# Kernel tuning notes

Measured on AMD Instinct MI355X. Metric: run time of the kernel, lower is better.

## Reference

```python
import jax, jax.numpy as jnp
import numpy as np

E = 400000
N = 100000
B = 64
D = 128          # token_dim
H = 128          # hidden_dim
A = 2 * H        # action_dim


def setup_inputs() -> dict:
    key = jax.random.key(0)
    ks = jax.random.split(key, 12)
    inp = {
        "relation_tokens": jax.random.normal(ks[0], (E, D), jnp.float32),
        "node_tokens": jax.random.normal(ks[1], (N, D), jnp.float32),
        "edge_index": jax.random.randint(ks[2], (2, E), 0, N, jnp.int64 if jax.config.jax_enable_x64 else jnp.int32),
        "question_tokens": jax.random.normal(ks[3], (B, D), jnp.float32),
        "edge_batch": jax.random.randint(ks[4], (E,), 0, B, jnp.int64 if jax.config.jax_enable_x64 else jnp.int32),
        # learned params (xavier-like small init); stored as [in, out] for x @ W
        "W_rel": jax.random.normal(ks[5], (D, H), jnp.float32) * 0.05,
        "W_node": jax.random.normal(ks[6], (D, H), jnp.float32) * 0.05,
        "W_qgate": jax.random.normal(ks[7], (D, A), jnp.float32) * 0.05,
        "W_mlp1": jax.random.normal(ks[8], (A, A), jnp.float32) * 0.05,
        "b_mlp1": jnp.zeros((A,), jnp.float32),
        "W_mlp2": jax.random.normal(ks[9], (A, A), jnp.float32) * 0.05,
        "b_mlp2": jnp.zeros((A,), jnp.float32),
    }
    return inp


def reference(relation_tokens, node_tokens, edge_index, question_tokens, edge_batch,
              W_rel, W_node, W_qgate, W_mlp1, b_mlp1, W_mlp2, b_mlp2):
    # TrajectoryAgent.precompute_action_keys (dropout=0 -> identity)
    tail_nodes = edge_index[1]                       # [E]
    tail_tokens = node_tokens[tail_nodes]            # gather -> [E, D]
    q_tokens = question_tokens[edge_batch]           # gather -> [E, D]

    rel_key = relation_tokens @ W_rel                # [E, H]
    node_key = tail_tokens @ W_node                  # [E, H]
    q_gate = jax.nn.sigmoid(q_tokens @ W_qgate)      # [E, 2H]

    action_key = jnp.concatenate((rel_key, node_key), axis=-1) * q_gate  # [E, 2H]

    # action_mlp: Linear -> exact GELU -> Linear (torch nn.GELU default = erf)
    h = jax.nn.gelu(action_key @ W_mlp1 + b_mlp1, approximate=False)
    return h @ W_mlp2 + b_mlp2                       # [E, 2H]
```

## Files before the change

kernel.cpp:

```cpp
#include <hip/hip_runtime.h>

typedef __bf16 bf16;
typedef bf16 bf16x4 __attribute__((ext_vector_type(4)));
typedef bf16 bf16x8 __attribute__((ext_vector_type(8)));
typedef float f32x4 __attribute__((ext_vector_type(4)));

#define WS_PK1   0
#define WS_PK2   32768
#define WS_PK3   98304
#define WS_QG    163840

__global__ void prep_weights(const float* __restrict__ Wrel,
                             const float* __restrict__ Wnode,
                             const float* __restrict__ W1,
                             const float* __restrict__ W2,
                             bf16* __restrict__ ws) {
  int id = blockIdx.x * 256 + threadIdx.x;
  if (id < 32768) {
    int cg = id >> 13, rem = id & 8191;
    int kk = rem >> 11;
    int ai = (rem >> 9) & 3;
    int l  = (rem >> 3) & 63;
    int j  = rem & 7;
    int n  = (cg & 1) * 64 + ai * 16 + (l & 15);
    int k  = kk * 32 + (l >> 4) * 8 + j;
    const float* src = (cg >> 1) ? Wnode : Wrel;
    ws[WS_PK1 + id] = (bf16)src[k * 128 + n];
  } else if (id < 98304) {
    int t = id - 32768;
    int cg = t >> 14, rem = t & 16383;
    int kk = rem >> 11;
    int ai = (rem >> 9) & 3;
    int l  = (rem >> 3) & 63;
    int j  = rem & 7;
    int n  = cg * 64 + ai * 16 + (l & 15);
    int k  = kk * 32 + (l >> 4) * 8 + j;
    ws[WS_PK2 + t] = (bf16)W1[k * 256 + n];
  } else if (id < 163840) {
    int t = id - 98304;
    int cg = t >> 14, rem = t & 16383;
    int kk = rem >> 11;
    int ai = (rem >> 9) & 3;
    int l  = (rem >> 3) & 63;
    int j  = rem & 7;
    int n  = cg * 64 + ai * 16 + (l & 15);
    int k  = kk * 32 + (l >> 4) * 8 + j;
    ws[WS_PK3 + t] = (bf16)W2[k * 256 + n];
  }
}

__global__ void prep_qg(const float* __restrict__ question,
                        const float* __restrict__ Wq,
                        bf16* __restrict__ qg) {
  int b = blockIdx.x, c = threadIdx.x;
  float s = 0.f;
#pragma unroll 8
  for (int k = 0; k < 128; ++k) s += question[b * 128 + k] * Wq[k * 256 + c];
  qg[b * 256 + c] = (bf16)(1.f / (1.f + expf(-s)));
}

__device__ __forceinline__ float gelu_fast(float x) {
  float x2 = x * x;
  float p = fmaf(0.0356774081f, x2, 0.7978845608f);
  float y = p * x;
  float e = __expf(2.f * y);
  float r = __builtin_amdgcn_rcpf(e + 1.f);
  float th = 1.f - 2.f * r;
  return 0.5f * x * (1.f + th);
}

typedef __attribute__((address_space(1))) const void gq_t;
typedef __attribute__((address_space(3))) void lq_t;
#define GLD16(g, s) __builtin_amdgcn_global_load_lds((gq_t*)(g), (lq_t*)(s), 16, 0, 0)
#define SBF() __builtin_amdgcn_sched_barrier(0xF)
#define SB7() __builtin_amdgcn_sched_barrier(0x7)
#define WAIT_VM0()   { asm volatile("s_waitcnt vmcnt(0)" ::: "memory"); SBF(); }
#define WAIT_LGKM0() { asm volatile("s_waitcnt lgkmcnt(0)" ::: "memory"); SBF(); }
#define VMWAIT(u)    { if ((u) <= 77)      { asm volatile("s_waitcnt vmcnt(2)" ::: "memory"); } \
                       else if ((u) == 78) { asm volatile("s_waitcnt vmcnt(1)" ::: "memory"); } \
                       else                { asm volatile("s_waitcnt vmcnt(0)" ::: "memory"); } \
                       SBF(); }
#define BAR() __builtin_amdgcn_s_barrier()

__global__ __launch_bounds__(256, 3) void fused_main(
    const float* __restrict__ rel_tok,
    const float* __restrict__ node_tok,
    const int*   __restrict__ tail_idx,
    const int*   __restrict__ ebatch,
    const bf16*  __restrict__ pk1,
    const bf16*  __restrict__ pk2,
    const bf16*  __restrict__ pk3,
    const bf16*  __restrict__ qg,
    const float* __restrict__ b1,
    const float* __restrict__ b2,
    float* __restrict__ out)
{
  __shared__ char  s_buf[32768];
  __shared__ char  s_w[16384];
  __shared__ float s_bias[512];

  const int tid = threadIdx.x;
  const int cg  = tid >> 6;
  const int l   = tid & 63;
  const int lo  = l & 15;
  const int hi  = l >> 4;
  const int base = blockIdx.x * 64;
  const int h1  = cg >> 1;

  auto issue_sub = [&](int u) {
    const bf16* g;
    if (u < 16)      g = pk1 + cg * 8192  + u * 512;
    else if (u < 48) g = pk2 + cg * 16384 + (u - 16) * 512;
    else             g = pk3 + cg * 16384 + (u - 48) * 512;
    GLD16(g + l * 8, s_w + (u & 3) * 4096 + cg * 1024 + l * 16);
  };

  int ebv[4];
#pragma unroll
  for (int bj = 0; bj < 4; ++bj) ebv[bj] = ebatch[base + bj * 16 + lo];
  bf16x4 gv[4][4];
#pragma unroll
  for (int bj = 0; bj < 4; ++bj)
#pragma unroll
    for (int ai = 0; ai < 4; ++ai)
      gv[bj][ai] = *(const bf16x4*)(qg + ebv[bj] * 256 + cg * 64 + ai * 16 + hi * 4);
  s_bias[tid]       = b1[tid];
  s_bias[256 + tid] = b2[tid];

  {
    const float4* g = (const float4*)rel_tok + (size_t)base * 32;
#pragma unroll
    for (int i = 0; i < 8; ++i) {
      int idx = tid + i * 256;
      int row = idx >> 5, c4 = idx & 31;
      float4 v = g[idx];
      bf16x4 b; b[0] = (bf16)v.x; b[1] = (bf16)v.y; b[2] = (bf16)v.z; b[3] = (bf16)v.w;
      int off = row * 256 + ((c4 * 8) ^ ((row & 15) << 4));
      *(bf16x4*)(s_buf + off) = b;
    }
#pragma unroll
    for (int i = 0; i < 8; ++i) {
      int idx = tid + i * 256;
      int row = idx >> 5, c4 = idx & 31;
      int tail = tail_idx[base + row];
      float4 v = ((const float4*)node_tok)[(size_t)tail * 32 + c4];
      bf16x4 b; b[0] = (bf16)v.x; b[1] = (bf16)v.y; b[2] = (bf16)v.z; b[3] = (bf16)v.w;
      int off = 16384 + row * 256 + ((c4 * 8) ^ ((row & 15) << 4));
      *(bf16x4*)(s_buf + off) = b;
    }
  }

  WAIT_VM0();
  issue_sub(0);
  issue_sub(1);
  issue_sub(2);
  WAIT_LGKM0();
  BAR();

  const f32x4 zero4 = {0.f, 0.f, 0.f, 0.f};
  const int wrd = cg * 1024 + l * 16;

  f32x4 acc1[4][4];
#pragma unroll
  for (int ai = 0; ai < 4; ++ai)
#pragma unroll
    for (int bj = 0; bj < 4; ++bj) acc1[ai][bj] = zero4;

#pragma unroll
  for (int kk = 0; kk < 4; ++kk) {
    bf16x8 bf[4];
#pragma unroll
    for (int bj = 0; bj < 4; ++bj) {
      int e = bj * 16 + lo;
      bf[bj] = *(const bf16x8*)(s_buf + h1 * 16384 + e * 256 +
                                ((kk * 64 + hi * 16) ^ ((e & 15) << 4)));
    }
#pragma unroll
    for (int ai = 0; ai < 4; ++ai) {
      const int u = kk * 4 + ai;
      VMWAIT(u);
      bf16x8 a = *(const bf16x8*)(s_w + (u & 3) * 4096 + wrd);
      __builtin_amdgcn_s_setprio(1);
#pragma unroll
      for (int bj = 0; bj < 4; ++bj)
        acc1[ai][bj] = __builtin_amdgcn_mfma_f32_16x16x32_bf16(a, bf[bj], acc1[ai][bj], 0, 0, 0);
      __builtin_amdgcn_s_setprio(0);
      SB7();
      issue_sub(u + 3);
    }
  }
  BAR();

#pragma unroll
  for (int bj = 0; bj < 4; ++bj) {
    int e = bj * 16 + lo;
#pragma unroll
    for (int ai = 0; ai < 4; ++ai) {
      int col0 = cg * 64 + ai * 16 + hi * 4;
      bf16x4 pk;
      pk[0] = (bf16)(acc1[ai][bj][0] * (float)gv[bj][ai][0]);
      pk[1] = (bf16)(acc1[ai][bj][1] * (float)gv[bj][ai][1]);
      pk[2] = (bf16)(acc1[ai][bj][2] * (float)gv[bj][ai][2]);
      pk[3] = (bf16)(acc1[ai][bj][3] * (float)gv[bj][ai][3]);
      int off = e * 512 + ((2 * col0) ^ ((e & 15) << 4));
      *(bf16x4*)(s_buf + off) = pk;
    }
  }
  WAIT_LGKM0();
  BAR();

  f32x4 acc2[4][4];
#pragma unroll
  for (int ai = 0; ai < 4; ++ai)
#pragma unroll
    for (int bj = 0; bj < 4; ++bj) acc2[ai][bj] = zero4;

#pragma unroll
  for (int kk = 0; kk < 8; ++kk) {
    bf16x8 bf[4];
#pragma unroll
    for (int bj = 0; bj < 4; ++bj) {
      int e = bj * 16 + lo;
      bf[bj] = *(const bf16x8*)(s_buf + e * 512 +
                                ((kk * 64 + hi * 16) ^ ((e & 15) << 4)));
    }
#pragma unroll
    for (int ai = 0; ai < 4; ++ai) {
      const int u = 16 + kk * 4 + ai;
      VMWAIT(u);
      bf16x8 a = *(const bf16x8*)(s_w + (u & 3) * 4096 + wrd);
      __builtin_amdgcn_s_setprio(1);
#pragma unroll
      for (int bj = 0; bj < 4; ++bj)
        acc2[ai][bj] = __builtin_amdgcn_mfma_f32_16x16x32_bf16(a, bf[bj], acc2[ai][bj], 0, 0, 0);
      __builtin_amdgcn_s_setprio(0);
      SB7();
      issue_sub(u + 3);
    }
  }
  BAR();

#pragma unroll
  for (int bj = 0; bj < 4; ++bj) {
    int e = bj * 16 + lo;
#pragma unroll
    for (int ai = 0; ai < 4; ++ai) {
      int col0 = cg * 64 + ai * 16 + hi * 4;
      float4 bv = *(const float4*)(s_bias + col0);
      bf16x4 pk;
      pk[0] = (bf16)gelu_fast(acc2[ai][bj][0] + bv.x);
      pk[1] = (bf16)gelu_fast(acc2[ai][bj][1] + bv.y);
      pk[2] = (bf16)gelu_fast(acc2[ai][bj][2] + bv.z);
      pk[3] = (bf16)gelu_fast(acc2[ai][bj][3] + bv.w);
      int off = e * 512 + ((2 * col0) ^ ((e & 15) << 4));
      *(bf16x4*)(s_buf + off) = pk;
    }
  }
  WAIT_LGKM0();
  BAR();

  f32x4 acc3[4][4];
#pragma unroll
  for (int ai = 0; ai < 4; ++ai)
#pragma unroll
    for (int bj = 0; bj < 4; ++bj) acc3[ai][bj] = zero4;

#pragma unroll
  for (int kk = 0; kk < 8; ++kk) {
    bf16x8 bf[4];
#pragma unroll
    for (int bj = 0; bj < 4; ++bj) {
      int e = bj * 16 + lo;
      bf[bj] = *(const bf16x8*)(s_buf + e * 512 +
                                ((kk * 64 + hi * 16) ^ ((e & 15) << 4)));
    }
#pragma unroll
    for (int ai = 0; ai < 4; ++ai) {
      const int u = 48 + kk * 4 + ai;
      VMWAIT(u);
      bf16x8 a = *(const bf16x8*)(s_w + (u & 3) * 4096 + wrd);
      __builtin_amdgcn_s_setprio(1);
#pragma unroll
      for (int bj = 0; bj < 4; ++bj)
        acc3[ai][bj] = __builtin_amdgcn_mfma_f32_16x16x32_bf16(a, bf[bj], acc3[ai][bj], 0, 0, 0);
      __builtin_amdgcn_s_setprio(0);
      if (u + 3 < 80) { SB7(); issue_sub(u + 3); }
    }
  }

#pragma unroll
  for (int bj = 0; bj < 4; ++bj) {
    int e = bj * 16 + lo;
#pragma unroll
    for (int ai = 0; ai < 4; ++ai) {
      int col0 = cg * 64 + ai * 16 + hi * 4;
      float4 bv = *(const float4*)(s_bias + 256 + col0);
      float4 o;
      o.x = acc3[ai][bj][0] + bv.x;
      o.y = acc3[ai][bj][1] + bv.y;
      o.z = acc3[ai][bj][2] + bv.z;
      o.w = acc3[ai][bj][3] + bv.w;
      *(float4*)(out + (size_t)(base + e) * 256 + col0) = o;
    }
  }
}

extern "C" void kernel_launch(void* const* d_in, const int* in_sizes, int n_in,
                              void* d_out, int out_size, void* d_ws, size_t ws_size,
                              hipStream_t stream) {
  const float* rel    = (const float*)d_in[0];
  const float* node   = (const float*)d_in[1];
  const int*   eidx   = (const int*)d_in[2];
  const float* quest  = (const float*)d_in[3];
  const int*   ebat   = (const int*)d_in[4];
  const float* Wrel   = (const float*)d_in[5];
  const float* Wnode  = (const float*)d_in[6];
  const float* Wq     = (const float*)d_in[7];
  const float* W1     = (const float*)d_in[8];
  const float* bias1  = (const float*)d_in[9];
  const float* W2     = (const float*)d_in[10];
  const float* bias2  = (const float*)d_in[11];
  float* outp = (float*)d_out;
  bf16* ws = (bf16*)d_ws;

  const int E = in_sizes[4];

  prep_weights<<<640, 256, 0, stream>>>(Wrel, Wnode, W1, W2, ws);
  prep_qg<<<64, 256, 0, stream>>>(quest, Wq, ws + WS_QG);
  fused_main<<<E / 64, 256, 0, stream>>>(
      rel, node, eidx + E, ebat,
      ws + WS_PK1, ws + WS_PK2, ws + WS_PK3, ws + WS_QG,
      bias1, bias2, outp);
}
```

Before: 285.4 us.

## Deepen weight prefetch ring and software-pipeline LDS operand reads ahead of MFMAs

Weight staging grows from a 4-slot to a 6-slot LDS ring with prefetch distance 4, and the next A fragment and next k-step B fragments are read from LDS one iteration ahead, so LDS latency overlaps with MFMA work. Occupancy hint drops from 3 to 2 blocks per CU to make room for the extra registers and LDS. The aim is to hide global-to-LDS and LDS-to-register latency in the three GEMM stages. The cost is fewer resident waves for latency hiding and more register pressure. Ring-slot reuse safety relies on the vmcnt waits and barriers lining up with the new distance.

```diff
diff --git a/kernel.cpp b/kernel.cpp
--- a/kernel.cpp
+++ b/kernel.cpp
@@ -76,13 +76,14 @@
 #define SB7() __builtin_amdgcn_sched_barrier(0x7)
 #define WAIT_VM0()   { asm volatile("s_waitcnt vmcnt(0)" ::: "memory"); SBF(); }
 #define WAIT_LGKM0() { asm volatile("s_waitcnt lgkmcnt(0)" ::: "memory"); SBF(); }
-#define VMWAIT(u)    { if ((u) <= 77)      { asm volatile("s_waitcnt vmcnt(2)" ::: "memory"); } \
-                       else if ((u) == 78) { asm volatile("s_waitcnt vmcnt(1)" ::: "memory"); } \
+#define VMWAITN(u)   { if ((u) <= 76)      { asm volatile("s_waitcnt vmcnt(2)" ::: "memory"); } \
+                       else if ((u) == 77) { asm volatile("s_waitcnt vmcnt(1)" ::: "memory"); } \
                        else                { asm volatile("s_waitcnt vmcnt(0)" ::: "memory"); } \
                        SBF(); }
+#define VMWAITP()    { asm volatile("s_waitcnt vmcnt(3)" ::: "memory"); SBF(); }
 #define BAR() __builtin_amdgcn_s_barrier()
 
-__global__ __launch_bounds__(256, 3) void fused_main(
+__global__ __launch_bounds__(256, 2) void fused_main(
     const float* __restrict__ rel_tok,
     const float* __restrict__ node_tok,
     const int*   __restrict__ tail_idx,
@@ -96,7 +97,7 @@
     float* __restrict__ out)
 {
   __shared__ char  s_buf[32768];
-  __shared__ char  s_w[16384];
+  __shared__ char  s_w[24576];
   __shared__ float s_bias[512];
 
   const int tid = threadIdx.x;
@@ -112,7 +113,7 @@
     if (u < 16)      g = pk1 + cg * 8192  + u * 512;
     else if (u < 48) g = pk2 + cg * 16384 + (u - 16) * 512;
     else             g = pk3 + cg * 16384 + (u - 48) * 512;
-    GLD16(g + l * 8, s_w + (u & 3) * 4096 + cg * 1024 + l * 16);
+    GLD16(g + l * 8, s_w + (u % 6) * 4096 + cg * 1024 + l * 16);
   };
 
   int ebv[4];
@@ -154,11 +155,16 @@
   issue_sub(0);
   issue_sub(1);
   issue_sub(2);
+  issue_sub(3);
   WAIT_LGKM0();
   BAR();
 
   const f32x4 zero4 = {0.f, 0.f, 0.f, 0.f};
   const int wrd = cg * 1024 + l * 16;
+#define READ_A(u) (*(const bf16x8*)(s_w + ((u) % 6) * 4096 + wrd))
+
+  bf16x8 a_cur, a_nxt;
+  bf16x8 bfc[4], bfn[4];
 
   f32x4 acc1[4][4];
 #pragma unroll
@@ -166,27 +172,42 @@
 #pragma unroll
     for (int bj = 0; bj < 4; ++bj) acc1[ai][bj] = zero4;
 
+  VMWAITP();
+  a_cur = READ_A(0);
+#pragma unroll
+  for (int bj = 0; bj < 4; ++bj) {
+    int e = bj * 16 + lo;
+    bfc[bj] = *(const bf16x8*)(s_buf + h1 * 16384 + e * 256 +
+                               ((hi * 16) ^ ((e & 15) << 4)));
+  }
+
 #pragma unroll
   for (int kk = 0; kk < 4; ++kk) {
-    bf16x8 bf[4];
-#pragma unroll
-    for (int bj = 0; bj < 4; ++bj) {
-      int e = bj * 16 + lo;
-      bf[bj] = *(const bf16x8*)(s_buf + h1 * 16384 + e * 256 +
-                                ((kk * 64 + hi * 16) ^ ((e & 15) << 4)));
-    }
 #pragma unroll
     for (int ai = 0; ai < 4; ++ai) {
       const int u = kk * 4 + ai;
-      VMWAIT(u);
-      bf16x8 a = *(const bf16x8*)(s_w + (u & 3) * 4096 + wrd);
+      VMWAITN(u);
+      a_nxt = READ_A(u + 1);
+      if (ai == 1 && kk < 3) {
+#pragma unroll
+        for (int bj = 0; bj < 4; ++bj) {
+          int e = bj * 16 + lo;
+          bfn[bj] = *(const bf16x8*)(s_buf + h1 * 16384 + e * 256 +
+                                     (((kk + 1) * 64 + hi * 16) ^ ((e & 15) << 4)));
+        }
+      }
       __builtin_amdgcn_s_setprio(1);
 #pragma unroll
       for (int bj = 0; bj < 4; ++bj)
-        acc1[ai][bj] = __builtin_amdgcn_mfma_f32_16x16x32_bf16(a, bf[bj], acc1[ai][bj], 0, 0, 0);
+        acc1[ai][bj] = __builtin_amdgcn_mfma_f32_16x16x32_bf16(a_cur, bfc[bj], acc1[ai][bj], 0, 0, 0);
       __builtin_amdgcn_s_setprio(0);
       SB7();
-      issue_sub(u + 3);
+      issue_sub(u + 4);
+      a_cur = a_nxt;
+    }
+    if (kk < 3) {
+#pragma unroll
+      for (int bj = 0; bj < 4; ++bj) bfc[bj] = bfn[bj];
     }
   }
   BAR();
@@ -216,26 +237,38 @@
     for (int bj = 0; bj < 4; ++bj) acc2[ai][bj] = zero4;
 
 #pragma unroll
+  for (int bj = 0; bj < 4; ++bj) {
+    int e = bj * 16 + lo;
+    bfc[bj] = *(const bf16x8*)(s_buf + e * 512 + ((hi * 16) ^ ((e & 15) << 4)));
+  }
+
+#pragma unroll
   for (int kk = 0; kk < 8; ++kk) {
-    bf16x8 bf[4];
-#pragma unroll
-    for (int bj = 0; bj < 4; ++bj) {
-      int e = bj * 16 + lo;
-      bf[bj] = *(const bf16x8*)(s_buf + e * 512 +
-                                ((kk * 64 + hi * 16) ^ ((e & 15) << 4)));
-    }
 #pragma unroll
     for (int ai = 0; ai < 4; ++ai) {
       const int u = 16 + kk * 4 + ai;
-      VMWAIT(u);
-      bf16x8 a = *(const bf16x8*)(s_w + (u & 3) * 4096 + wrd);
+      VMWAITN(u);
+      a_nxt = READ_A(u + 1);
+      if (ai == 1 && kk < 7) {
+#pragma unroll
+        for (int bj = 0; bj < 4; ++bj) {
+          int e = bj * 16 + lo;
+          bfn[bj] = *(const bf16x8*)(s_buf + e * 512 +
+                                     (((kk + 1) * 64 + hi * 16) ^ ((e & 15) << 4)));
+        }
+      }
       __builtin_amdgcn_s_setprio(1);
 #pragma unroll
       for (int bj = 0; bj < 4; ++bj)
-        acc2[ai][bj] = __builtin_amdgcn_mfma_f32_16x16x32_bf16(a, bf[bj], acc2[ai][bj], 0, 0, 0);
+        acc2[ai][bj] = __builtin_amdgcn_mfma_f32_16x16x32_bf16(a_cur, bfc[bj], acc2[ai][bj], 0, 0, 0);
       __builtin_amdgcn_s_setprio(0);
       SB7();
-      issue_sub(u + 3);
+      issue_sub(u + 4);
+      a_cur = a_nxt;
+    }
+    if (kk < 7) {
+#pragma unroll
+      for (int bj = 0; bj < 4; ++bj) bfc[bj] = bfn[bj];
     }
   }
   BAR();
@@ -266,25 +299,39 @@
     for (int bj = 0; bj < 4; ++bj) acc3[ai][bj] = zero4;
 
 #pragma unroll
+  for (int bj = 0; bj < 4; ++bj) {
+    int e = bj * 16 + lo;
+    bfc[bj] = *(const bf16x8*)(s_buf + e * 512 + ((hi * 16) ^ ((e & 15) << 4)));
+  }
+
+#pragma unroll
   for (int kk = 0; kk < 8; ++kk) {
-    bf16x8 bf[4];
-#pragma unroll
-    for (int bj = 0; bj < 4; ++bj) {
-      int e = bj * 16 + lo;
-      bf[bj] = *(const bf16x8*)(s_buf + e * 512 +
-                                ((kk * 64 + hi * 16) ^ ((e & 15) << 4)));
-    }
 #pragma unroll
     for (int ai = 0; ai < 4; ++ai) {
       const int u = 48 + kk * 4 + ai;
-      VMWAIT(u);
-      bf16x8 a = *(const bf16x8*)(s_w + (u & 3) * 4096 + wrd);
+      if (u < 79) {
+        VMWAITN(u);
+        a_nxt = READ_A(u + 1);
+      }
+      if (ai == 1 && kk < 7) {
+#pragma unroll
+        for (int bj = 0; bj < 4; ++bj) {
+          int e = bj * 16 + lo;
+          bfn[bj] = *(const bf16x8*)(s_buf + e * 512 +
+                                     (((kk + 1) * 64 + hi * 16) ^ ((e & 15) << 4)));
+        }
+      }
       __builtin_amdgcn_s_setprio(1);
 #pragma unroll
       for (int bj = 0; bj < 4; ++bj)
-        acc3[ai][bj] = __builtin_amdgcn_mfma_f32_16x16x32_bf16(a, bf[bj], acc3[ai][bj], 0, 0, 0);
+        acc3[ai][bj] = __builtin_amdgcn_mfma_f32_16x16x32_bf16(a_cur, bfc[bj], acc3[ai][bj], 0, 0, 0);
       __builtin_amdgcn_s_setprio(0);
-      if (u + 3 < 80) { SB7(); issue_sub(u + 3); }
+      if (u + 4 < 80) { SB7(); issue_sub(u + 4); }
+      a_cur = a_nxt;
+    }
+    if (kk < 7) {
+#pragma unroll
+      for (int bj = 0; bj < 4; ++bj) bfc[bj] = bfn[bj];
     }
   }
 
```

After: 325.8 us. 14.1% more time.
